# Kernel optimization log

Hardware: AMD Instinct MI355X
Metric: run time of the kernel (lower is better)

Reference implementation:

```python
import jax, jax.numpy as jnp
import numpy as np

N, E, IN_DIM, OUT_DIM, R = 50000, 800000, 128, 128, 8


def setup_inputs() -> dict:
    key = jax.random.key(0)
    k1, k2, k3, k4, k5 = jax.random.split(key, 5)
    x = jax.random.normal(k1, (N, IN_DIM), dtype=jnp.float32)
    edge_index = jax.random.randint(k2, (2, E), 0, N, dtype=jnp.int32)
    edge_type = jax.random.randint(k3, (E,), 0, R, dtype=jnp.int32)
    # Xavier-uniform-ish init for parameters
    lim_w = float(np.sqrt(6.0 / (IN_DIM + OUT_DIM)))
    weight = jax.random.uniform(k4, (R, IN_DIM, OUT_DIM), dtype=jnp.float32, minval=-lim_w, maxval=lim_w)
    self_weight = jax.random.uniform(k5, (IN_DIM, OUT_DIM), dtype=jnp.float32, minval=-lim_w, maxval=lim_w)
    return {"x": x, "weight": weight, "self_weight": self_weight,
            "edge_index": edge_index, "edge_type": edge_type}


def reference(x, weight, self_weight, edge_index, edge_type):
    n = x.shape[0]
    r = weight.shape[0]
    d_out = weight.shape[2]
    src, dst = edge_index[0], edge_index[1]
    # undirected: symmetrize edges (directed=False)
    src_all = jnp.concatenate([src, dst])          # [2E]
    dst_all = jnp.concatenate([dst, src])          # [2E]
    et_all = jnp.concatenate([edge_type, edge_type])  # [2E]
    # transform all nodes by every relation weight once: [R, N, D_out]
    xw = jnp.einsum('ni,rio->rno', x, weight)
    # gather per-edge messages already transformed by their relation's W_r
    msg = xw[et_all, src_all]                      # [2E, D_out]
    # fused (relation, dst) segment id -> per-relation scatter-add
    seg = et_all.astype(jnp.int32) * n + dst_all
    agg = jax.ops.segment_sum(msg, seg, num_segments=r * n).reshape(r, n, d_out)
    deg = jax.ops.segment_sum(jnp.ones_like(seg, dtype=x.dtype), seg,
                              num_segments=r * n).reshape(r, n)
    deg_inv = jnp.where(deg > 0, 1.0 / jnp.maximum(deg, 1.0), jnp.zeros_like(deg))
    out = jnp.sum(agg * deg_inv[..., None], axis=0)  # [N, D_out]
    out = out + x @ self_weight                       # self-loop
    return out
```

## Files before the change

### kernel.cpp

```cpp
#include <hip/hip_runtime.h>

#define NN 50000
#define EE 800000
#define RR 8
#define DD 128
#define SS (NN*RR)
#define TE (2*EE)
#define NB 782
#define NBLK 391
#define NS (NB*NBLK)

typedef __attribute__((ext_vector_type(8))) short bf16x8;
typedef __attribute__((ext_vector_type(4))) float f32x4;

__device__ __forceinline__ unsigned short f2bf(float f){
  unsigned int u = __float_as_uint(f);
  u += 0x7fffu + ((u >> 16) & 1u);
  return (unsigned short)(u >> 16);
}
__device__ __forceinline__ float bf_lo(unsigned int w){ return __uint_as_float(w << 16); }
__device__ __forceinline__ float bf_hi(unsigned int w){ return __uint_as_float(w & 0xffff0000u); }

__device__ __forceinline__ void acc8(float* a, uint4 u){
  a[0] += bf_lo(u.x); a[1] += bf_hi(u.x);
  a[2] += bf_lo(u.y); a[3] += bf_hi(u.y);
  a[4] += bf_lo(u.z); a[5] += bf_hi(u.z);
  a[6] += bf_lo(u.w); a[7] += bf_hi(u.w);
}
__device__ __forceinline__ unsigned int pack2(float a, float b){
  return ((unsigned int)f2bf(b) << 16) | (unsigned int)f2bf(a);
}

__device__ __forceinline__ void dir_edge(const int* ei, const int* et, int j,
                                         int& s, int& d, int& t){
  if (j < EE){ s = ei[j]; d = ei[EE + j]; t = et[j]; }
  else { int jj = j - EE; s = ei[EE + jj]; d = ei[jj]; t = et[jj]; }
}

__global__ __launch_bounds__(256) void k_hist(const int* __restrict__ ei,
                                              const int* __restrict__ et,
                                              int* __restrict__ hist){
  __shared__ int h[NB];
  int tid = threadIdx.x, bid = blockIdx.x;
  for (int i = tid; i < NB; i += 256) h[i] = 0;
  __syncthreads();
  int j0 = bid*4096;
  for (int k = tid; k < 4096; k += 256){
    int j = j0 + k;
    if (j < TE){
      int s, d, t; dir_edge(ei, et, j, s, d, t);
      atomicAdd(&h[d >> 6], 1);
    }
  }
  __syncthreads();
  for (int i = tid; i < NB; i += 256) hist[i*NBLK + bid] = h[i];
}

__global__ __launch_bounds__(256) void k_scan1(int* __restrict__ hist,
                                               int* __restrict__ blksum){
  __shared__ int sd[256];
  int b = blockIdx.x, tid = threadIdx.x;
  int base = b*1024 + tid*4;
  int v0 = (base+0 < NS) ? hist[base+0] : 0;
  int v1 = (base+1 < NS) ? hist[base+1] : 0;
  int v2 = (base+2 < NS) ? hist[base+2] : 0;
  int v3 = (base+3 < NS) ? hist[base+3] : 0;
  int ts = v0+v1+v2+v3;
  sd[tid] = ts; __syncthreads();
  for (int o = 1; o < 256; o <<= 1){
    int t = (tid >= o) ? sd[tid-o] : 0;
    __syncthreads();
    sd[tid] += t;
    __syncthreads();
  }
  int ex = sd[tid] - ts;
  if (base+0 < NS) hist[base+0] = ex; ex += v0;
  if (base+1 < NS) hist[base+1] = ex; ex += v1;
  if (base+2 < NS) hist[base+2] = ex; ex += v2;
  if (base+3 < NS) hist[base+3] = ex;
  if (tid == 255) blksum[b] = sd[255];
}

__global__ __launch_bounds__(512) void k_scan2(int* __restrict__ blksum, int nb){
  __shared__ int sd[512];
  int tid = threadIdx.x;
  int v = (tid < nb) ? blksum[tid] : 0;
  sd[tid] = v; __syncthreads();
  for (int o = 1; o < 512; o <<= 1){
    int t = (tid >= o) ? sd[tid-o] : 0;
    __syncthreads();
    sd[tid] += t;
    __syncthreads();
  }
  if (tid < nb) blksum[tid] = sd[tid] - v;
}

__global__ __launch_bounds__(256) void k_scan3(int* __restrict__ hist,
                                               const int* __restrict__ blksum){
  int i = blockIdx.x*blockDim.x + threadIdx.x;
  if (i < NS) hist[i] += blksum[i >> 10];
}

__global__ __launch_bounds__(256) void k_part(const int* __restrict__ ei,
                                              const int* __restrict__ et,
                                              const int* __restrict__ S,
                                              unsigned int* __restrict__ P){
  __shared__ int cur[NB];
  int tid = threadIdx.x, bid = blockIdx.x;
  for (int i = tid; i < NB; i += 256) cur[i] = S[i*NBLK + bid];
  __syncthreads();
  int j0 = bid*4096;
  for (int k = tid; k < 4096; k += 256){
    int j = j0 + k;
    if (j < TE){
      int s, d, t; dir_edge(ei, et, j, s, d, t);
      int b = d >> 6;
      int p = atomicAdd(&cur[b], 1);
      P[p] = (unsigned int)s | ((unsigned int)(d & 63) << 17)
           | ((unsigned int)t << 23);
    }
  }
}

__global__ __launch_bounds__(256) void k_build(const unsigned int* __restrict__ P,
                                               const int* __restrict__ S,
                                               int* __restrict__ esrc,
                                               int* __restrict__ offs){
  __shared__ int h[512], cu[512], sd[256];
  int tid = threadIdx.x, b = blockIdx.x;
  int pstart = S[b*NBLK];
  int pend   = (b+1 < NB) ? S[(b+1)*NBLK] : TE;
  int ne = pend - pstart;
  h[2*tid] = 0; h[2*tid+1] = 0;
  __syncthreads();
  for (int k = tid; k < ne; k += 256){
    unsigned int u = P[pstart + k];
    int lseg = (int)(((u >> 17) & 63u)*8u + (u >> 23));
    atomicAdd(&h[lseg], 1);
  }
  __syncthreads();
  int v0 = h[2*tid], v1 = h[2*tid+1];
  int ts = v0 + v1;
  sd[tid] = ts; __syncthreads();
  for (int o = 1; o < 256; o <<= 1){
    int t = (tid >= o) ? sd[tid-o] : 0;
    __syncthreads();
    sd[tid] += t;
    __syncthreads();
  }
  int ex = sd[tid] - ts;
  cu[2*tid]   = pstart + ex;
  cu[2*tid+1] = pstart + ex + v0;
  int seg0 = b*512;
  if (seg0 + 2*tid     < SS) offs[seg0 + 2*tid]     = cu[2*tid];
  if (seg0 + 2*tid + 1 < SS) offs[seg0 + 2*tid + 1] = cu[2*tid+1];
  if (b == NB-1 && tid == 0) offs[SS] = TE;
  __syncthreads();
  for (int k = tid; k < ne; k += 256){
    unsigned int u = P[pstart + k];
    int lseg = (int)(((u >> 17) & 63u)*8u + (u >> 23));
    int r = atomicAdd(&cu[lseg], 1);
    esrc[r] = (int)(u & 0x1ffffu);
  }
}

__global__ __launch_bounds__(256) void k_conv(const float* __restrict__ x,
                                              const float* __restrict__ w,
                                              const float* __restrict__ sw,
                                              unsigned short* __restrict__ xb,
                                              unsigned short* __restrict__ wb){
  int i = blockIdx.x*blockDim.x + threadIdx.x;
  const int M1 = NN*DD/4;
  if (i < M1){
    float4 v = ((const float4*)x)[i];
    ushort4 o;
    o.x = f2bf(v.x); o.y = f2bf(v.y); o.z = f2bf(v.z); o.w = f2bf(v.w);
    ((ushort4*)xb)[i] = o;
  } else {
    int j = i - M1;
    if (j < 9*DD*DD){
      int r = j >> 14; int rem = j & 16383; int n = rem >> 7; int k = rem & 127;
      float v = (r < 8) ? w[r*16384 + k*128 + n] : sw[k*128 + n];
      wb[j] = f2bf(v);
    }
  }
}

__global__ __launch_bounds__(256) void k_fused(
    const unsigned short* __restrict__ xb,
    const unsigned short* __restrict__ wb,
    const int* __restrict__ offs,
    const int* __restrict__ esrc,
    float* __restrict__ out)
{
  __shared__ __align__(16) unsigned short Alds[2][32][136];
  const int tid  = threadIdx.x;
  const int wave = tid >> 6, lane = tid & 63;
  const int l15  = lane & 15, quad = lane >> 4;
  const int g    = quad;
  const int gl   = l15;
  const int gbase = g << 4;
  const int rowbase = blockIdx.x * 32;

  f32x4 C[2][2];
  #pragma unroll
  for (int m = 0; m < 2; ++m){ C[m][0] = (f32x4)(0.f); C[m][1] = (f32x4)(0.f); }

  auto gather = [&](int rr, int b){
    int v = 0;
    if (rr < 8 && lane < 16){
      int gdj = rowbase + wave*8 + (lane >> 1);
      if (gdj < NN) v = offs[gdj*8 + rr + (lane & 1)];
    }
    #pragma unroll
    for (int p = 0; p < 2; ++p){
      int rl8  = 2*g + p;
      int rowl = wave*8 + rl8;
      int gd   = rowbase + rowl;
      uint4 u = make_uint4(0u,0u,0u,0u);
      if (rr == 8){
        if (gd < NN) u = *(const uint4*)(xb + (size_t)gd*DD + gl*8);
      } else {
        int off = __shfl(v, 2*rl8);
        int end = __shfl(v, 2*rl8 + 1);
        int cnt = (gd < NN) ? (end - off) : 0;
        float a[8] = {0.f,0.f,0.f,0.f,0.f,0.f,0.f,0.f};
        int idxv = 0;
        if (gl < cnt) idxv = esrc[off + gl];
        int cm = cnt < 16 ? cnt : 16;
        int e = 0;
        for (; e + 4 <= cm; e += 4){
          int s0 = __shfl(idxv, gbase + e + 0);
          int s1 = __shfl(idxv, gbase + e + 1);
          int s2 = __shfl(idxv, gbase + e + 2);
          int s3 = __shfl(idxv, gbase + e + 3);
          uint4 u0 = *(const uint4*)(xb + (size_t)s0*DD + gl*8);
          uint4 u1 = *(const uint4*)(xb + (size_t)s1*DD + gl*8);
          uint4 u2 = *(const uint4*)(xb + (size_t)s2*DD + gl*8);
          uint4 u3 = *(const uint4*)(xb + (size_t)s3*DD + gl*8);
          acc8(a, u0); acc8(a, u1); acc8(a, u2); acc8(a, u3);
        }
        for (; e < cm; ++e){
          int s0 = __shfl(idxv, gbase + e);
          uint4 u0 = *(const uint4*)(xb + (size_t)s0*DD + gl*8);
          acc8(a, u0);
        }
        for (int e2 = 16; e2 < cnt; ++e2){
          int s0 = esrc[off + e2];
          uint4 u0 = *(const uint4*)(xb + (size_t)s0*DD + gl*8);
          acc8(a, u0);
        }
        float sc = (cnt > 0) ? (1.0f / (float)cnt) : 0.f;
        u.x = pack2(a[0]*sc, a[1]*sc);
        u.y = pack2(a[2]*sc, a[3]*sc);
        u.z = pack2(a[4]*sc, a[5]*sc);
        u.w = pack2(a[6]*sc, a[7]*sc);
      }
      *(uint4*)&Alds[b][rowl][gl*8] = u;
    }
  };

  gather(0, 0);
  __syncthreads();

  #pragma unroll 1
  for (int rr = 0; rr < 9; ++rr){
    int b = rr & 1;
    if (rr < 8) gather(rr + 1, b ^ 1);

    const unsigned short* wr = wb + rr * 16384;
    bf16x8 bfrag[2][4];
    #pragma unroll
    for (int nt = 0; nt < 2; ++nt)
      #pragma unroll
      for (int ks = 0; ks < 4; ++ks)
        bfrag[nt][ks] = *(const bf16x8*)(wr + (wave*32 + nt*16 + l15)*128 + ks*32 + quad*8);

    #pragma unroll
    for (int m = 0; m < 2; ++m){
      #pragma unroll
      for (int ks = 0; ks < 4; ++ks){
        bf16x8 af = *(const bf16x8*)&Alds[b][m*16 + l15][ks*32 + quad*8];
        C[m][0] = __builtin_amdgcn_mfma_f32_16x16x32_bf16(af, bfrag[0][ks], C[m][0], 0, 0, 0);
        C[m][1] = __builtin_amdgcn_mfma_f32_16x16x32_bf16(af, bfrag[1][ks], C[m][1], 0, 0, 0);
      }
    }
    __syncthreads();
  }

  #pragma unroll
  for (int m = 0; m < 2; ++m){
    #pragma unroll
    for (int nt = 0; nt < 2; ++nt){
      #pragma unroll
      for (int i = 0; i < 4; ++i){
        int row = m*16 + quad*4 + i;
        int gd  = rowbase + row;
        int col = wave*32 + nt*16 + l15;
        if (gd < NN) out[gd*DD + col] = C[m][nt][i];
      }
    }
  }
}

extern "C" void kernel_launch(void* const* d_in, const int* in_sizes, int n_in,
                              void* d_out, int out_size, void* d_ws, size_t ws_size,
                              hipStream_t stream){
  const float* x  = (const float*)d_in[0];
  const float* w  = (const float*)d_in[1];
  const float* sw = (const float*)d_in[2];
  const int*   ei = (const int*)d_in[3];
  const int*   et = (const int*)d_in[4];
  float* out = (float*)d_out;
  char* ws = (char*)d_ws;

  if (ws_size < (size_t)21100000) return;

  unsigned short* xb = (unsigned short*)(ws + 0);
  int*          hist = (int*)(ws + 0);
  int*        blksum = (int*)(ws + 1223168);
  unsigned int*    P = (unsigned int*)(ws + 1225216);
  int*          esrc = (int*)(ws + 12800000);
  int*          offs = (int*)(ws + 19200000);
  unsigned short* wb = (unsigned short*)(ws + 20800016);

  k_hist <<<NBLK, 256, 0, stream>>>(ei, et, hist);
  k_scan1<<<(NS + 1023)/1024, 256, 0, stream>>>(hist, blksum);
  k_scan2<<<1, 512, 0, stream>>>(blksum, (NS + 1023)/1024);
  k_scan3<<<(NS + 255)/256, 256, 0, stream>>>(hist, blksum);
  k_part <<<NBLK, 256, 0, stream>>>(ei, et, hist, P);
  k_build<<<NB, 256, 0, stream>>>(P, hist, esrc, offs);
  k_conv <<<(NN*DD/4 + 9*DD*DD + 255)/256, 256, 0, stream>>>(x, w, sw, xb, wb);
  k_fused<<<(NN + 31)/32, 256, 0, stream>>>(xb, wb, offs, esrc, out);
}
```

Measured before the change: 259.4 us.

## Fuse bf16 conversion into histogram, halve chunk and row tiles, stage partition in LDS

Folds the fp32-to-bf16 conversion of x and the weights into the histogram kernel, which removes one launch. Edge chunks shrink from 4096 to 2048 so the histogram and partition kernels run twice as many blocks. The build kernel now stages each bucket's packed edges in LDS instead of reading them from global memory twice. The fused gather+MFMA kernel processes 16 destination rows per block instead of 32, giving about 3125 blocks for better occupancy and load balance, but each wave does less MFMA work per weight-fragment load. The workspace layout is rearranged so P aliases esrc, which the build kernel relies on being safe because it reads P into LDS first.

```diff
diff --git a/kernel.cpp b/kernel.cpp
--- a/kernel.cpp
+++ b/kernel.cpp
@@ -7,8 +7,11 @@
 #define SS (NN*RR)
 #define TE (2*EE)
 #define NB 782
-#define NBLK 391
-#define NS (NB*NBLK)
+#define NBK 782
+#define CH 2048
+#define NS (NB*NBK)
+#define NSB 598
+#define MAXB 2816
 
 typedef __attribute__((ext_vector_type(8))) short bf16x8;
 typedef __attribute__((ext_vector_type(4))) float f32x4;
@@ -39,13 +42,18 @@
 
 __global__ __launch_bounds__(256) void k_hist(const int* __restrict__ ei,
                                               const int* __restrict__ et,
-                                              int* __restrict__ hist){
+                                              int* __restrict__ hist,
+                                              const float* __restrict__ x,
+                                              const float* __restrict__ w,
+                                              const float* __restrict__ sw,
+                                              unsigned short* __restrict__ xb,
+                                              unsigned short* __restrict__ wb){
   __shared__ int h[NB];
   int tid = threadIdx.x, bid = blockIdx.x;
   for (int i = tid; i < NB; i += 256) h[i] = 0;
   __syncthreads();
-  int j0 = bid*4096;
-  for (int k = tid; k < 4096; k += 256){
+  int j0 = bid*CH;
+  for (int k = tid; k < CH; k += 256){
     int j = j0 + k;
     if (j < TE){
       int s, d, t; dir_edge(ei, et, j, s, d, t);
@@ -53,7 +61,23 @@
     }
   }
   __syncthreads();
-  for (int i = tid; i < NB; i += 256) hist[i*NBLK + bid] = h[i];
+  for (int i = tid; i < NB; i += 256) hist[i*NBK + bid] = h[i];
+
+  const int M1 = NN*DD/4;
+  const int GT = NBK*256;
+  for (int i = bid*256 + tid; i < M1 + 9*DD*DD; i += GT){
+    if (i < M1){
+      float4 v = ((const float4*)x)[i];
+      ushort4 o;
+      o.x = f2bf(v.x); o.y = f2bf(v.y); o.z = f2bf(v.z); o.w = f2bf(v.w);
+      ((ushort4*)xb)[i] = o;
+    } else {
+      int j = i - M1;
+      int r = j >> 14; int rem = j & 16383; int n = rem >> 7; int kk = rem & 127;
+      float v = (r < 8) ? w[r*16384 + kk*128 + n] : sw[kk*128 + n];
+      wb[j] = f2bf(v);
+    }
+  }
 }
 
 __global__ __launch_bounds__(256) void k_scan1(int* __restrict__ hist,
@@ -81,12 +105,12 @@
   if (tid == 255) blksum[b] = sd[255];
 }
 
-__global__ __launch_bounds__(512) void k_scan2(int* __restrict__ blksum, int nb){
-  __shared__ int sd[512];
+__global__ __launch_bounds__(640) void k_scan2(int* __restrict__ blksum, int nb){
+  __shared__ int sd[640];
   int tid = threadIdx.x;
   int v = (tid < nb) ? blksum[tid] : 0;
   sd[tid] = v; __syncthreads();
-  for (int o = 1; o < 512; o <<= 1){
+  for (int o = 1; o < 640; o <<= 1){
     int t = (tid >= o) ? sd[tid-o] : 0;
     __syncthreads();
     sd[tid] += t;
@@ -107,10 +131,10 @@
                                               unsigned int* __restrict__ P){
   __shared__ int cur[NB];
   int tid = threadIdx.x, bid = blockIdx.x;
-  for (int i = tid; i < NB; i += 256) cur[i] = S[i*NBLK + bid];
-  __syncthreads();
-  int j0 = bid*4096;
-  for (int k = tid; k < 4096; k += 256){
+  for (int i = tid; i < NB; i += 256) cur[i] = S[i*NBK + bid];
+  __syncthreads();
+  int j0 = bid*CH;
+  for (int k = tid; k < CH; k += 256){
     int j = j0 + k;
     if (j < TE){
       int s, d, t; dir_edge(ei, et, j, s, d, t);
@@ -126,15 +150,17 @@
                                                const int* __restrict__ S,
                                                int* __restrict__ esrc,
                                                int* __restrict__ offs){
+  __shared__ unsigned int Pl[MAXB];
   __shared__ int h[512], cu[512], sd[256];
   int tid = threadIdx.x, b = blockIdx.x;
-  int pstart = S[b*NBLK];
-  int pend   = (b+1 < NB) ? S[(b+1)*NBLK] : TE;
+  int pstart = S[b*NBK];
+  int pend   = (b+1 < NB) ? S[(b+1)*NBK] : TE;
   int ne = pend - pstart;
   h[2*tid] = 0; h[2*tid+1] = 0;
+  for (int k = tid; k < ne && k < MAXB; k += 256) Pl[k] = P[pstart + k];
   __syncthreads();
   for (int k = tid; k < ne; k += 256){
-    unsigned int u = P[pstart + k];
+    unsigned int u = (k < MAXB) ? Pl[k] : P[pstart + k];
     int lseg = (int)(((u >> 17) & 63u)*8u + (u >> 23));
     atomicAdd(&h[lseg], 1);
   }
@@ -157,32 +183,10 @@
   if (b == NB-1 && tid == 0) offs[SS] = TE;
   __syncthreads();
   for (int k = tid; k < ne; k += 256){
-    unsigned int u = P[pstart + k];
+    unsigned int u = (k < MAXB) ? Pl[k] : P[pstart + k];
     int lseg = (int)(((u >> 17) & 63u)*8u + (u >> 23));
     int r = atomicAdd(&cu[lseg], 1);
     esrc[r] = (int)(u & 0x1ffffu);
-  }
-}
-
-__global__ __launch_bounds__(256) void k_conv(const float* __restrict__ x,
-                                              const float* __restrict__ w,
-                                              const float* __restrict__ sw,
-                                              unsigned short* __restrict__ xb,
-                                              unsigned short* __restrict__ wb){
-  int i = blockIdx.x*blockDim.x + threadIdx.x;
-  const int M1 = NN*DD/4;
-  if (i < M1){
-    float4 v = ((const float4*)x)[i];
-    ushort4 o;
-    o.x = f2bf(v.x); o.y = f2bf(v.y); o.z = f2bf(v.z); o.w = f2bf(v.w);
-    ((ushort4*)xb)[i] = o;
-  } else {
-    int j = i - M1;
-    if (j < 9*DD*DD){
-      int r = j >> 14; int rem = j & 16383; int n = rem >> 7; int k = rem & 127;
-      float v = (r < 8) ? w[r*16384 + k*128 + n] : sw[k*128 + n];
-      wb[j] = f2bf(v);
-    }
   }
 }
 
@@ -193,71 +197,65 @@
     const int* __restrict__ esrc,
     float* __restrict__ out)
 {
-  __shared__ __align__(16) unsigned short Alds[2][32][136];
+  __shared__ __align__(16) unsigned short Alds[2][16][136];
   const int tid  = threadIdx.x;
   const int wave = tid >> 6, lane = tid & 63;
   const int l15  = lane & 15, quad = lane >> 4;
   const int g    = quad;
   const int gl   = l15;
   const int gbase = g << 4;
-  const int rowbase = blockIdx.x * 32;
-
-  f32x4 C[2][2];
-  #pragma unroll
-  for (int m = 0; m < 2; ++m){ C[m][0] = (f32x4)(0.f); C[m][1] = (f32x4)(0.f); }
+  const int rowbase = blockIdx.x * 16;
+
+  f32x4 C0 = (f32x4)(0.f), C1 = (f32x4)(0.f);
 
   auto gather = [&](int rr, int b){
     int v = 0;
-    if (rr < 8 && lane < 16){
-      int gdj = rowbase + wave*8 + (lane >> 1);
+    if (rr < 8 && lane < 8){
+      int gdj = rowbase + wave*4 + (lane >> 1);
       if (gdj < NN) v = offs[gdj*8 + rr + (lane & 1)];
     }
-    #pragma unroll
-    for (int p = 0; p < 2; ++p){
-      int rl8  = 2*g + p;
-      int rowl = wave*8 + rl8;
-      int gd   = rowbase + rowl;
-      uint4 u = make_uint4(0u,0u,0u,0u);
-      if (rr == 8){
-        if (gd < NN) u = *(const uint4*)(xb + (size_t)gd*DD + gl*8);
-      } else {
-        int off = __shfl(v, 2*rl8);
-        int end = __shfl(v, 2*rl8 + 1);
-        int cnt = (gd < NN) ? (end - off) : 0;
-        float a[8] = {0.f,0.f,0.f,0.f,0.f,0.f,0.f,0.f};
-        int idxv = 0;
-        if (gl < cnt) idxv = esrc[off + gl];
-        int cm = cnt < 16 ? cnt : 16;
-        int e = 0;
-        for (; e + 4 <= cm; e += 4){
-          int s0 = __shfl(idxv, gbase + e + 0);
-          int s1 = __shfl(idxv, gbase + e + 1);
-          int s2 = __shfl(idxv, gbase + e + 2);
-          int s3 = __shfl(idxv, gbase + e + 3);
-          uint4 u0 = *(const uint4*)(xb + (size_t)s0*DD + gl*8);
-          uint4 u1 = *(const uint4*)(xb + (size_t)s1*DD + gl*8);
-          uint4 u2 = *(const uint4*)(xb + (size_t)s2*DD + gl*8);
-          uint4 u3 = *(const uint4*)(xb + (size_t)s3*DD + gl*8);
-          acc8(a, u0); acc8(a, u1); acc8(a, u2); acc8(a, u3);
-        }
-        for (; e < cm; ++e){
-          int s0 = __shfl(idxv, gbase + e);
-          uint4 u0 = *(const uint4*)(xb + (size_t)s0*DD + gl*8);
-          acc8(a, u0);
-        }
-        for (int e2 = 16; e2 < cnt; ++e2){
-          int s0 = esrc[off + e2];
-          uint4 u0 = *(const uint4*)(xb + (size_t)s0*DD + gl*8);
-          acc8(a, u0);
-        }
-        float sc = (cnt > 0) ? (1.0f / (float)cnt) : 0.f;
-        u.x = pack2(a[0]*sc, a[1]*sc);
-        u.y = pack2(a[2]*sc, a[3]*sc);
-        u.z = pack2(a[4]*sc, a[5]*sc);
-        u.w = pack2(a[6]*sc, a[7]*sc);
+    int rowl = wave*4 + g;
+    int gd   = rowbase + rowl;
+    uint4 u = make_uint4(0u,0u,0u,0u);
+    if (rr == 8){
+      if (gd < NN) u = *(const uint4*)(xb + (size_t)gd*DD + gl*8);
+    } else {
+      int off = __shfl(v, 2*g);
+      int end = __shfl(v, 2*g + 1);
+      int cnt = (gd < NN) ? (end - off) : 0;
+      float a[8] = {0.f,0.f,0.f,0.f,0.f,0.f,0.f,0.f};
+      int idxv = 0;
+      if (gl < cnt) idxv = esrc[off + gl];
+      int cm = cnt < 16 ? cnt : 16;
+      int e = 0;
+      for (; e + 4 <= cm; e += 4){
+        int s0 = __shfl(idxv, gbase + e + 0);
+        int s1 = __shfl(idxv, gbase + e + 1);
+        int s2 = __shfl(idxv, gbase + e + 2);
+        int s3 = __shfl(idxv, gbase + e + 3);
+        uint4 u0 = *(const uint4*)(xb + (size_t)s0*DD + gl*8);
+        uint4 u1 = *(const uint4*)(xb + (size_t)s1*DD + gl*8);
+        uint4 u2 = *(const uint4*)(xb + (size_t)s2*DD + gl*8);
+        uint4 u3 = *(const uint4*)(xb + (size_t)s3*DD + gl*8);
+        acc8(a, u0); acc8(a, u1); acc8(a, u2); acc8(a, u3);
       }
-      *(uint4*)&Alds[b][rowl][gl*8] = u;
-    }
+      for (; e < cm; ++e){
+        int s0 = __shfl(idxv, gbase + e);
+        uint4 u0 = *(const uint4*)(xb + (size_t)s0*DD + gl*8);
+        acc8(a, u0);
+      }
+      for (int e2 = 16; e2 < cnt; ++e2){
+        int s0 = esrc[off + e2];
+        uint4 u0 = *(const uint4*)(xb + (size_t)s0*DD + gl*8);
+        acc8(a, u0);
+      }
+      float sc = (cnt > 0) ? (1.0f / (float)cnt) : 0.f;
+      u.x = pack2(a[0]*sc, a[1]*sc);
+      u.y = pack2(a[2]*sc, a[3]*sc);
+      u.z = pack2(a[4]*sc, a[5]*sc);
+      u.w = pack2(a[6]*sc, a[7]*sc);
+    }
+    *(uint4*)&Alds[b][rowl][gl*8] = u;
   };
 
   gather(0, 0);
@@ -277,28 +275,21 @@
         bfrag[nt][ks] = *(const bf16x8*)(wr + (wave*32 + nt*16 + l15)*128 + ks*32 + quad*8);
 
     #pragma unroll
-    for (int m = 0; m < 2; ++m){
-      #pragma unroll
-      for (int ks = 0; ks < 4; ++ks){
-        bf16x8 af = *(const bf16x8*)&Alds[b][m*16 + l15][ks*32 + quad*8];
-        C[m][0] = __builtin_amdgcn_mfma_f32_16x16x32_bf16(af, bfrag[0][ks], C[m][0], 0, 0, 0);
-        C[m][1] = __builtin_amdgcn_mfma_f32_16x16x32_bf16(af, bfrag[1][ks], C[m][1], 0, 0, 0);
-      }
+    for (int ks = 0; ks < 4; ++ks){
+      bf16x8 af = *(const bf16x8*)&Alds[b][l15][ks*32 + quad*8];
+      C0 = __builtin_amdgcn_mfma_f32_16x16x32_bf16(af, bfrag[0][ks], C0, 0, 0, 0);
+      C1 = __builtin_amdgcn_mfma_f32_16x16x32_bf16(af, bfrag[1][ks], C1, 0, 0, 0);
     }
     __syncthreads();
   }
 
   #pragma unroll
-  for (int m = 0; m < 2; ++m){
-    #pragma unroll
-    for (int nt = 0; nt < 2; ++nt){
-      #pragma unroll
-      for (int i = 0; i < 4; ++i){
-        int row = m*16 + quad*4 + i;
-        int gd  = rowbase + row;
-        int col = wave*32 + nt*16 + l15;
-        if (gd < NN) out[gd*DD + col] = C[m][nt][i];
-      }
+  for (int i = 0; i < 4; ++i){
+    int row = quad*4 + i;
+    int gd  = rowbase + row;
+    if (gd < NN){
+      out[gd*DD + wave*32 +      l15] = C0[i];
+      out[gd*DD + wave*32 + 16 + l15] = C1[i];
     }
   }
 }
@@ -314,22 +305,21 @@
   float* out = (float*)d_out;
   char* ws = (char*)d_ws;
 
-  if (ws_size < (size_t)21100000) return;
+  if (ws_size < (size_t)23550000) return;
 
   unsigned short* xb = (unsigned short*)(ws + 0);
-  int*          hist = (int*)(ws + 0);
-  int*        blksum = (int*)(ws + 1223168);
-  unsigned int*    P = (unsigned int*)(ws + 1225216);
+  unsigned int*    P = (unsigned int*)(ws + 12800000);
   int*          esrc = (int*)(ws + 12800000);
   int*          offs = (int*)(ws + 19200000);
   unsigned short* wb = (unsigned short*)(ws + 20800016);
-
-  k_hist <<<NBLK, 256, 0, stream>>>(ei, et, hist);
-  k_scan1<<<(NS + 1023)/1024, 256, 0, stream>>>(hist, blksum);
-  k_scan2<<<1, 512, 0, stream>>>(blksum, (NS + 1023)/1024);
+  int*          hist = (int*)(ws + 21094928);
+  int*        blksum = (int*)(ws + 23541024);
+
+  k_hist <<<NBK, 256, 0, stream>>>(ei, et, hist, x, w, sw, xb, wb);
+  k_scan1<<<NSB, 256, 0, stream>>>(hist, blksum);
+  k_scan2<<<1, 640, 0, stream>>>(blksum, NSB);
   k_scan3<<<(NS + 255)/256, 256, 0, stream>>>(hist, blksum);
-  k_part <<<NBLK, 256, 0, stream>>>(ei, et, hist, P);
+  k_part <<<NBK, 256, 0, stream>>>(ei, et, hist, P);
   k_build<<<NB, 256, 0, stream>>>(P, hist, esrc, offs);
-  k_conv <<<(NN*DD/4 + 9*DD*DD + 255)/256, 256, 0, stream>>>(x, w, sw, xb, wb);
-  k_fused<<<(NN + 31)/32, 256, 0, stream>>>(xb, wb, offs, esrc, out);
-}
+  k_fused<<<(NN + 15)/16, 256, 0, stream>>>(xb, wb, offs, esrc, out);
+}
```

New measurement: 291.5 us. 1.12x slower.
